# Optimization experiments

Measured on AMD Instinct MI355X. Metric: run time of the kernel, lower is better.

## Reference

```python
import jax, jax.numpy as jnp
import numpy as np

EPS = 0.01    # halting threshold eps
MU = 2.0      # halting probability multiplier
N_MAX = 16    # static upper bound on ACT steps (loop halts in 1-2 steps w/ bias=1, mu=2)

# Binarize: hard threshold at 1-eps forward, straight-through (identity) backward
@jax.custom_vjp
def binarize(x):
    return (x >= 1.0 - EPS).astype(x.dtype)

def _bin_fwd(x):
    return binarize(x), None

def _bin_bwd(_, g):
    return (g,)

binarize.defvjp(_bin_fwd, _bin_bwd)


def setup_inputs() -> dict:
    key = jax.random.key(0)
    ks = jax.random.split(key, 12)
    I, H, O = 4095, 4096, 4096
    sc = 1.0 / np.sqrt(H)
    u = lambda k, s: jax.random.uniform(k, s, jnp.float32, -sc, sc)
    return {
        "x": jax.random.normal(ks[0], (I,), jnp.float32),
        "s0": jax.random.normal(ks[1], (H,), jnp.float32) * 0.1,
        "y0": jax.random.normal(ks[2], (O,), jnp.float32),
        "h0": jnp.zeros((1,), jnp.float32),
        # nn.RNN (tanh) single layer params
        "W_ih": u(ks[3], (H, 1 + I)),
        "b_ih": u(ks[4], (H,)),
        "W_hh": u(ks[5], (H, H)),
        "b_hh": u(ks[6], (H,)),
        # fc_halt (bias hard-set to 1.0 in __init__)
        "W_halt": u(ks[7], (1, H)),
        "b_halt": jnp.ones((1,), jnp.float32),
        # fc_output
        "W_out": u(ks[8], (O, H)),
        "b_out": u(ks[9], (O,)),
    }


def reference(x, s0, y0, h0, W_ih, b_ih, W_hh, b_hh, W_halt, b_halt, W_out, b_out):
    x0 = jnp.concatenate([jnp.zeros((1,), x.dtype), x])  # skip-flag 0 input
    x1 = jnp.concatenate([jnp.ones((1,), x.dtype), x])   # skip-flag 1 input (first step)

    def step(carry, t):
        s, acc = carry
        xin = jnp.where(t == 0, x1, x0)
        valid = acc[0] < 1.0 - EPS  # ACT while-loop condition at step start
        s_new = jnp.tanh(W_ih @ xin + b_ih + W_hh @ s + b_hh)  # tanh RNN cell
        y_new = W_out @ s_new + b_out
        acc_new = acc + MU * jax.nn.sigmoid(W_halt @ s_new + b_halt)
        s_next = jnp.where(valid, s_new, s)
        acc_next = jnp.where(valid, acc_new, acc)
        return (s_next, acc_next), (s_new, y_new, acc_new, valid)

    (_, _), (S, Y, A, V) = jax.lax.scan(step, (s0, h0), jnp.arange(N_MAX))
    # S:[T,H]  Y:[T,O]  A:[T,1]  V:[T] bool
    vmask = V.astype(x.dtype)                 # steps the ACT loop actually executed
    bin_acc = binarize(A[:, 0])               # 0 before halting step, 1 at/after
    halt_bin = bin_acc * vmask                # exactly 1 at the halting step n
    h0_bin = binarize(h0)[0]
    y_sel = jnp.einsum('to,t->o', Y, halt_bin)   # torch.mv(outputs_tensor, bin)
    s_sel = jnp.einsum('th,t->h', S, halt_bin)
    output = h0_bin * y0 + (1.0 - h0_bin) * y_sel
    s = h0_bin * s0 + (1.0 - h0_bin) * s_sel
    ponder = (1.0 - h0_bin) * jnp.sum(vmask * (1.0 - bin_acc))   # = n-1, or 0 if no steps
    last_acc = h0_bin * h0 + (1.0 - h0_bin) * jnp.sum(halt_bin * A[:, 0])[None]
    return (output, s, ponder, last_acc - 1.0)
```

## Files before the change

kernel.cpp:

```cpp
#include <hip/hip_runtime.h>
#include <math.h>


#define H      4096
#define NMAX   16
#define THRESH 0.99f

__device__ __forceinline__ float wave_reduce(float a) {
    #pragma unroll
    for (int off = 32; off > 0; off >>= 1) a += __shfl_down(a, off);
    return a;
}

__global__ __launch_bounds__(256) void k_prep(
    const float* __restrict__ x, float* __restrict__ ws, float* __restrict__ out)
{
    const int i = blockIdx.x * 256 + threadIdx.x;
    if (i < 32) ws[i] = 0.f;
    if (i == 0) out[H] = 0.f;
    if (i < H - 1) out[H + 1 + i] = x[i];
}

__global__ __launch_bounds__(256, 8) void k_step0(
    const float* __restrict__ s0,     const float* __restrict__ h0,
    const float* __restrict__ W_ih,   const float* __restrict__ b_ih,
    const float* __restrict__ W_hh,   const float* __restrict__ b_hh,
    const float* __restrict__ W_halt,
    float* __restrict__ ws, float* __restrict__ out)
{
    if (h0[0] >= THRESH) return;

    const int tid  = threadIdx.x, bid = blockIdx.x;
    const int wave = tid >> 6,   lane = tid & 63;
    const int row  = (bid << 1) + (wave >> 1);
    const int base = ((wave & 1) << 9) + lane;

    const float4* wi4 = (const float4*)(W_ih + (size_t)row * H);
    const float4* wh4 = (const float4*)(W_hh + (size_t)row * H);
    const float4* xv4 = (const float4*)(out + H);
    const float4* sv4 = (const float4*)s0;

    float4 wa[8];
    #pragma unroll
    for (int k = 0; k < 8; ++k) wa[k] = wi4[base + (k << 6)];
    float a0 = 0.f;
    #pragma unroll
    for (int k = 0; k < 8; ++k) {
        float4 xv = xv4[base + (k << 6)];
        a0 += wa[k].x*xv.x + wa[k].y*xv.y + wa[k].z*xv.z + wa[k].w*xv.w;
    }
    float4 wb[8];
    #pragma unroll
    for (int k = 0; k < 8; ++k) wb[k] = wh4[base + (k << 6)];
    float a1 = 0.f;
    #pragma unroll
    for (int k = 0; k < 8; ++k) {
        float4 sv = sv4[base + (k << 6)];
        a1 += wb[k].x*sv.x + wb[k].y*sv.y + wb[k].z*sv.z + wb[k].w*sv.w;
    }

    float a = wave_reduce(a0 + a1);
    __shared__ float part[4];
    if (lane == 0) part[wave] = a;
    __syncthreads();
    if (tid == 0) {
        const int r0 = bid << 1, r1 = r0 + 1;
        float z0 = part[0] + part[1] + b_ih[r0] + b_hh[r0] + W_ih[(size_t)r0 * H];
        float z1 = part[2] + part[3] + b_ih[r1] + b_hh[r1] + W_ih[(size_t)r1 * H];
        float s1a = tanhf(z0), s1b = tanhf(z1);
        ws[32 + r0] = s1a;
        ws[32 + r1] = s1b;
        out[r0] = W_halt[r0] * s1a;
        out[r1] = W_halt[r1] * s1b;
    }
}

#define RG   256
#define RT   256

__device__ __forceinline__ void grid_barrier(int* cnt, int* gen) {
    __syncthreads();
    if (threadIdx.x == 0) {
        __threadfence();
        int g = __hip_atomic_load(gen, __ATOMIC_RELAXED, __HIP_MEMORY_SCOPE_AGENT);
        int prev = __hip_atomic_fetch_add(cnt, 1, __ATOMIC_ACQ_REL, __HIP_MEMORY_SCOPE_AGENT);
        if (prev == RG - 1) {
            __hip_atomic_store(cnt, 0, __ATOMIC_RELAXED, __HIP_MEMORY_SCOPE_AGENT);
            __hip_atomic_fetch_add(gen, 1, __ATOMIC_RELEASE, __HIP_MEMORY_SCOPE_AGENT);
        } else {
            while (__hip_atomic_load(gen, __ATOMIC_ACQUIRE, __HIP_MEMORY_SCOPE_AGENT) == g)
                __builtin_amdgcn_s_sleep(8);
        }
        __threadfence();
    }
    __syncthreads();
}

__global__ __launch_bounds__(RT) void k_rest(
    const float* __restrict__ x,
    const float* __restrict__ h0,
    const float* __restrict__ W_ih,   const float* __restrict__ b_ih,
    const float* __restrict__ W_hh,   const float* __restrict__ b_hh,
    const float* __restrict__ W_halt, const float* __restrict__ b_halt,
    const float* __restrict__ hpart,  float* ws)
{
    int* wsI = (int*)ws;
    if (h0[0] >= THRESH) return;

    const int tid = threadIdx.x, bid = blockIdx.x;
    const int wave = tid >> 6, lane = tid & 63;

    {
        const float4* p4 = (const float4*)hpart;
        float a = 0.f;
        #pragma unroll
        for (int j = 0; j < 4; ++j) {
            float4 v = p4[tid + (j << 8)];
            a += v.x + v.y + v.z + v.w;
        }
        a = wave_reduce(a);
        __shared__ float pr[4];
        if (lane == 0) pr[wave] = a;
        __syncthreads();
        float hd  = pr[0] + pr[1] + pr[2] + pr[3];
        float sg  = 1.f / (1.f + expf(-(hd + b_halt[0])));
        float acc0 = h0[0] + 2.f * sg;
        if (acc0 >= THRESH) {
            if (bid == 0 && tid == 0) {
                wsI[4] = 1; wsI[5] = 0; wsI[6] = 0; ws[8] = acc0;
            }
            return;
        }
        if (bid == 0 && tid == 0) { wsI[4] = 0; }
        __syncthreads();
    }

    float* hdot = ws + 16;
    float* sb0  = ws + 32;
    float* sb1  = ws + 32 + H;

    __shared__ float xl[H];
    __shared__ float sl[H];
    if (tid == 0) xl[0] = 0.f;
    for (int i = tid; i < H - 1; i += RT) xl[i + 1] = x[i];

    float acc;
    {
        const float4* p4 = (const float4*)hpart;
        float a = 0.f;
        #pragma unroll
        for (int j = 0; j < 4; ++j) {
            float4 v = p4[tid + (j << 8)];
            a += v.x + v.y + v.z + v.w;
        }
        a = wave_reduce(a);
        __shared__ float pr2[4];
        if (lane == 0) pr2[wave] = a;
        __syncthreads();
        float hd = pr2[0] + pr2[1] + pr2[2] + pr2[3];
        acc = h0[0] + 2.f / (1.f + expf(-(hd + b_halt[0])));
    }
    int   ponder = 1;
    const float bh = b_halt[0];
    bool  halted = false;
    int   sel = 0;
    float last_acc = 0.f;

    for (int t = 1; t < NMAX; ++t) {
        const float* scur = (t & 1) ? sb0 : sb1;
        float*       snew = (t & 1) ? sb1 : sb0;

        __syncthreads();
        for (int i = tid; i < H / 4; i += RT)
            ((float4*)sl)[i] = ((const float4*)scur)[i];
        __syncthreads();

        for (int r = 0; r < 4; ++r) {
            const int row = bid * 16 + r * 4 + wave;
            const float4* wih = (const float4*)(W_ih + (size_t)row * H);
            const float4* whh = (const float4*)(W_hh + (size_t)row * H);
            float a0 = 0.f, a1 = 0.f;
            #pragma unroll 4
            for (int k = 0; k < 16; ++k) {
                const int idx = lane + (k << 6);
                float4 wa = wih[idx], wb = whh[idx];
                float4 va = ((const float4*)xl)[idx], vb = ((const float4*)sl)[idx];
                a0 += wa.x*va.x + wa.y*va.y + wa.z*va.z + wa.w*va.w;
                a1 += wb.x*vb.x + wb.y*vb.y + wb.z*vb.z + wb.w*vb.w;
            }
            float a = wave_reduce(a0 + a1);
            if (lane == 0) {
                float sv = tanhf(a + b_ih[row] + b_hh[row]);
                snew[row] = sv;
                atomicAdd(&hdot[t], W_halt[row] * sv);
            }
        }

        grid_barrier((int*)ws, (int*)ws + 1);

        float hd = ((volatile float*)hdot)[t];
        float sg = 1.f / (1.f + expf(-(hd + bh)));
        acc += 2.f * sg;
        if (acc >= THRESH) { halted = true; last_acc = acc; sel = (t & 1) ? 1 : 0; break; }
        ponder++;
    }

    if (bid == 0 && tid == 0) {
        wsI[4] = halted ? 1 : 0;
        wsI[5] = sel;
        wsI[6] = ponder;
        ws[8]  = last_acc;
    }
}

__global__ __launch_bounds__(256, 8) void k_out(
    const float* __restrict__ s0,    const float* __restrict__ y0,
    const float* __restrict__ h0,
    const float* __restrict__ W_out, const float* __restrict__ b_out,
    const float* __restrict__ ws, float* __restrict__ out)
{
    const float h0v = h0[0];
    const int tid = threadIdx.x, bid = blockIdx.x;

    if (h0v >= THRESH) {
        const int i = bid * 256 + tid;
        if (i < H) { out[i] = y0[i]; out[H + i] = s0[i]; }
        if (i == 0) { out[2*H] = 0.f; out[2*H + 1] = h0v - 1.f; }
        return;
    }

    const int* wsI = (const int*)ws;
    if (!wsI[4]) {
        const int i = bid * 256 + tid;
        if (i < H) { out[i] = 0.f; out[H + i] = 0.f; }
        if (i == 0) { out[2*H] = (float)wsI[6]; out[2*H + 1] = -1.f; }
        return;
    }

    const float* sfin = ws + 32 + (wsI[5] ? H : 0);
    const int wave = tid >> 6, lane = tid & 63;
    const int row  = (bid << 1) + (wave >> 1);
    const int base = ((wave & 1) << 9) + lane;

    const float4* w4 = (const float4*)(W_out + (size_t)row * H);
    const float4* v4 = (const float4*)sfin;

    float4 wa[8];
    #pragma unroll
    for (int k = 0; k < 8; ++k) wa[k] = w4[base + (k << 6)];
    float a0 = 0.f;
    #pragma unroll
    for (int k = 0; k < 8; ++k) {
        float4 vv = v4[base + (k << 6)];
        a0 += wa[k].x*vv.x + wa[k].y*vv.y + wa[k].z*vv.z + wa[k].w*vv.w;
    }

    float a = wave_reduce(a0);
    __shared__ float part[4];
    if (lane == 0) part[wave] = a;
    __syncthreads();
    if (tid == 0) {
        const int r0 = bid << 1, r1 = r0 + 1;
        out[r0]     = part[0] + part[1] + b_out[r0];
        out[r1]     = part[2] + part[3] + b_out[r1];
        out[H + r0] = sfin[r0];
        out[H + r1] = sfin[r1];
        if (bid == 0) {
            out[2*H]     = (float)wsI[6];
            out[2*H + 1] = ws[8] - 1.f;
        }
    }
}

extern "C" void kernel_launch(void* const* d_in, const int* in_sizes, int n_in,
                              void* d_out, int out_size, void* d_ws, size_t ws_size,
                              hipStream_t stream) {
    const float* x      = (const float*)d_in[0];
    const float* s0     = (const float*)d_in[1];
    const float* y0     = (const float*)d_in[2];
    const float* h0     = (const float*)d_in[3];
    const float* W_ih   = (const float*)d_in[4];
    const float* b_ih   = (const float*)d_in[5];
    const float* W_hh   = (const float*)d_in[6];
    const float* b_hh   = (const float*)d_in[7];
    const float* W_halt = (const float*)d_in[8];
    const float* b_halt = (const float*)d_in[9];
    const float* W_out  = (const float*)d_in[10];
    const float* b_out  = (const float*)d_in[11];
    float* out = (float*)d_out;
    float* ws  = (float*)d_ws;

    k_prep<<<dim3(16),   dim3(256), 0, stream>>>(x, ws, out);
    k_step0<<<dim3(2048), dim3(256), 0, stream>>>(
        s0, h0, W_ih, b_ih, W_hh, b_hh, W_halt, ws, out);
    k_rest<<<dim3(RG),   dim3(RT),  0, stream>>>(
        x, h0, W_ih, b_ih, W_hh, b_hh, W_halt, b_halt, out, ws);
    k_out<<<dim3(2048),  dim3(256), 0, stream>>>(
        s0, y0, h0, W_out, b_out, ws, out);
}
```

Before: 224.6 us.

## Fuse step0, recurrent steps and output projection into one persistent kernel

```diff
diff --git a/kernel.cpp b/kernel.cpp
--- a/kernel.cpp
+++ b/kernel.cpp
@@ -5,78 +5,14 @@
 #define H      4096
 #define NMAX   16
 #define THRESH 0.99f
+#define RG     1024
+#define RT     256
 
 __device__ __forceinline__ float wave_reduce(float a) {
     #pragma unroll
     for (int off = 32; off > 0; off >>= 1) a += __shfl_down(a, off);
     return a;
 }
-
-__global__ __launch_bounds__(256) void k_prep(
-    const float* __restrict__ x, float* __restrict__ ws, float* __restrict__ out)
-{
-    const int i = blockIdx.x * 256 + threadIdx.x;
-    if (i < 32) ws[i] = 0.f;
-    if (i == 0) out[H] = 0.f;
-    if (i < H - 1) out[H + 1 + i] = x[i];
-}
-
-__global__ __launch_bounds__(256, 8) void k_step0(
-    const float* __restrict__ s0,     const float* __restrict__ h0,
-    const float* __restrict__ W_ih,   const float* __restrict__ b_ih,
-    const float* __restrict__ W_hh,   const float* __restrict__ b_hh,
-    const float* __restrict__ W_halt,
-    float* __restrict__ ws, float* __restrict__ out)
-{
-    if (h0[0] >= THRESH) return;
-
-    const int tid  = threadIdx.x, bid = blockIdx.x;
-    const int wave = tid >> 6,   lane = tid & 63;
-    const int row  = (bid << 1) + (wave >> 1);
-    const int base = ((wave & 1) << 9) + lane;
-
-    const float4* wi4 = (const float4*)(W_ih + (size_t)row * H);
-    const float4* wh4 = (const float4*)(W_hh + (size_t)row * H);
-    const float4* xv4 = (const float4*)(out + H);
-    const float4* sv4 = (const float4*)s0;
-
-    float4 wa[8];
-    #pragma unroll
-    for (int k = 0; k < 8; ++k) wa[k] = wi4[base + (k << 6)];
-    float a0 = 0.f;
-    #pragma unroll
-    for (int k = 0; k < 8; ++k) {
-        float4 xv = xv4[base + (k << 6)];
-        a0 += wa[k].x*xv.x + wa[k].y*xv.y + wa[k].z*xv.z + wa[k].w*xv.w;
-    }
-    float4 wb[8];
-    #pragma unroll
-    for (int k = 0; k < 8; ++k) wb[k] = wh4[base + (k << 6)];
-    float a1 = 0.f;
-    #pragma unroll
-    for (int k = 0; k < 8; ++k) {
-        float4 sv = sv4[base + (k << 6)];
-        a1 += wb[k].x*sv.x + wb[k].y*sv.y + wb[k].z*sv.z + wb[k].w*sv.w;
-    }
-
-    float a = wave_reduce(a0 + a1);
-    __shared__ float part[4];
-    if (lane == 0) part[wave] = a;
-    __syncthreads();
-    if (tid == 0) {
-        const int r0 = bid << 1, r1 = r0 + 1;
-        float z0 = part[0] + part[1] + b_ih[r0] + b_hh[r0] + W_ih[(size_t)r0 * H];
-        float z1 = part[2] + part[3] + b_ih[r1] + b_hh[r1] + W_ih[(size_t)r1 * H];
-        float s1a = tanhf(z0), s1b = tanhf(z1);
-        ws[32 + r0] = s1a;
-        ws[32 + r1] = s1b;
-        out[r0] = W_halt[r0] * s1a;
-        out[r1] = W_halt[r1] * s1b;
-    }
-}
-
-#define RG   256
-#define RT   256
 
 __device__ __forceinline__ void grid_barrier(int* cnt, int* gen) {
     __syncthreads();
@@ -96,53 +32,83 @@
     __syncthreads();
 }
 
-__global__ __launch_bounds__(RT) void k_rest(
-    const float* __restrict__ x,
+__global__ __launch_bounds__(256) void k_prep(
+    const float* __restrict__ x, float* __restrict__ ws, float* __restrict__ out)
+{
+    const int i = blockIdx.x * 256 + threadIdx.x;
+    if (i < 32) ws[i] = 0.f;
+    if (i == 0) out[H] = 0.f;
+    if (i < H - 1) out[H + 1 + i] = x[i];
+}
+
+__global__ __launch_bounds__(RT, 4) void k_main(
+    const float* __restrict__ s0,    const float* __restrict__ y0,
     const float* __restrict__ h0,
-    const float* __restrict__ W_ih,   const float* __restrict__ b_ih,
-    const float* __restrict__ W_hh,   const float* __restrict__ b_hh,
-    const float* __restrict__ W_halt, const float* __restrict__ b_halt,
-    const float* __restrict__ hpart,  float* ws)
+    const float* __restrict__ W_ih,  const float* __restrict__ b_ih,
+    const float* __restrict__ W_hh,  const float* __restrict__ b_hh,
+    const float* __restrict__ W_halt,const float* __restrict__ b_halt,
+    const float* __restrict__ W_out, const float* __restrict__ b_out,
+    float* ws, float* __restrict__ out)
 {
-    int* wsI = (int*)ws;
-    if (h0[0] >= THRESH) return;
-
-    const int tid = threadIdx.x, bid = blockIdx.x;
+    const int tid  = threadIdx.x, bid = blockIdx.x;
+    const float h0v = h0[0];
+
+    if (h0v >= THRESH) {
+        const int i = bid * RT + tid;
+        if (i < H) { out[i] = y0[i]; out[H + i] = s0[i]; }
+        if (i == 0) { out[2*H] = 0.f; out[2*H + 1] = h0v - 1.f; }
+        return;
+    }
+
     const int wave = tid >> 6, lane = tid & 63;
+    const int row  = (bid << 2) + wave;
+
+    float* sb0   = ws + 32;
+    float* sb1   = ws + 32 + H;
+    float* hpart = ws + 32 + 2 * H;
+    float* hdot  = ws + 16;
+
+    const float4* wi4 = (const float4*)(W_ih + (size_t)row * H);
+    const float4* wh4 = (const float4*)(W_hh + (size_t)row * H);
+    const float4* xv4 = (const float4*)(out + H);
+    const float4* sv4 = (const float4*)s0;
+
+    const float bi  = b_ih[row];
+    const float bhh = b_hh[row];
+    const float w0c = W_ih[(size_t)row * H];
+    const float whl = W_halt[row];
+    const float bha = b_halt[0];
 
     {
-        const float4* p4 = (const float4*)hpart;
-        float a = 0.f;
+        float a0 = 0.f, a1 = 0.f;
+        float4 wreg[8];
         #pragma unroll
-        for (int j = 0; j < 4; ++j) {
-            float4 v = p4[tid + (j << 8)];
-            a += v.x + v.y + v.z + v.w;
-        }
-        a = wave_reduce(a);
-        __shared__ float pr[4];
-        if (lane == 0) pr[wave] = a;
-        __syncthreads();
-        float hd  = pr[0] + pr[1] + pr[2] + pr[3];
-        float sg  = 1.f / (1.f + expf(-(hd + b_halt[0])));
-        float acc0 = h0[0] + 2.f * sg;
-        if (acc0 >= THRESH) {
-            if (bid == 0 && tid == 0) {
-                wsI[4] = 1; wsI[5] = 0; wsI[6] = 0; ws[8] = acc0;
-            }
-            return;
-        }
-        if (bid == 0 && tid == 0) { wsI[4] = 0; }
-        __syncthreads();
-    }
-
-    float* hdot = ws + 16;
-    float* sb0  = ws + 32;
-    float* sb1  = ws + 32 + H;
-
-    __shared__ float xl[H];
-    __shared__ float sl[H];
-    if (tid == 0) xl[0] = 0.f;
-    for (int i = tid; i < H - 1; i += RT) xl[i + 1] = x[i];
+        for (int hseg = 0; hseg < 2; ++hseg) {
+            const int off = hseg << 9;
+            #pragma unroll
+            for (int k = 0; k < 8; ++k) wreg[k] = wi4[off + lane + (k << 6)];
+            #pragma unroll
+            for (int k = 0; k < 8; ++k) {
+                float4 v = xv4[off + lane + (k << 6)];
+                a0 += wreg[k].x*v.x + wreg[k].y*v.y + wreg[k].z*v.z + wreg[k].w*v.w;
+            }
+            #pragma unroll
+            for (int k = 0; k < 8; ++k) wreg[k] = wh4[off + lane + (k << 6)];
+            #pragma unroll
+            for (int k = 0; k < 8; ++k) {
+                float4 v = sv4[off + lane + (k << 6)];
+                a1 += wreg[k].x*v.x + wreg[k].y*v.y + wreg[k].z*v.z + wreg[k].w*v.w;
+            }
+        }
+        float a = wave_reduce(a0 + a1);
+        if (lane == 0) {
+            float s1 = tanhf(a + bi + bhh + w0c);
+            sb0[row]   = s1;
+            hpart[row] = whl * s1;
+        }
+    }
+
+    grid_barrier((int*)ws, (int*)ws + 1);
 
     float acc;
     {
@@ -154,121 +120,84 @@
             a += v.x + v.y + v.z + v.w;
         }
         a = wave_reduce(a);
-        __shared__ float pr2[4];
-        if (lane == 0) pr2[wave] = a;
+        __shared__ float pr[4];
+        if (lane == 0) pr[wave] = a;
         __syncthreads();
-        float hd = pr2[0] + pr2[1] + pr2[2] + pr2[3];
-        acc = h0[0] + 2.f / (1.f + expf(-(hd + b_halt[0])));
-    }
-    int   ponder = 1;
-    const float bh = b_halt[0];
-    bool  halted = false;
-    int   sel = 0;
-    float last_acc = 0.f;
-
-    for (int t = 1; t < NMAX; ++t) {
-        const float* scur = (t & 1) ? sb0 : sb1;
-        float*       snew = (t & 1) ? sb1 : sb0;
-
-        __syncthreads();
-        for (int i = tid; i < H / 4; i += RT)
-            ((float4*)sl)[i] = ((const float4*)scur)[i];
-        __syncthreads();
-
-        for (int r = 0; r < 4; ++r) {
-            const int row = bid * 16 + r * 4 + wave;
-            const float4* wih = (const float4*)(W_ih + (size_t)row * H);
-            const float4* whh = (const float4*)(W_hh + (size_t)row * H);
+        float hd = pr[0] + pr[1] + pr[2] + pr[3];
+        acc = h0v + 2.f / (1.f + expf(-(hd + bha)));
+    }
+
+    bool  halted;
+    int   sel = 0, ponder = 0;
+    float last_acc;
+
+    if (acc >= THRESH) {
+        halted = true; last_acc = acc;
+    } else {
+        halted = false; last_acc = 0.f; ponder = 1;
+        for (int t = 1; t < NMAX; ++t) {
+            const float* scur = (t & 1) ? sb0 : sb1;
+            float*       snew = (t & 1) ? sb1 : sb0;
+            const float4* sc4 = (const float4*)scur;
+
             float a0 = 0.f, a1 = 0.f;
             #pragma unroll 4
             for (int k = 0; k < 16; ++k) {
                 const int idx = lane + (k << 6);
-                float4 wa = wih[idx], wb = whh[idx];
-                float4 va = ((const float4*)xl)[idx], vb = ((const float4*)sl)[idx];
+                float4 wa = wi4[idx], wb = wh4[idx];
+                float4 va = xv4[idx], vb = sc4[idx];
                 a0 += wa.x*va.x + wa.y*va.y + wa.z*va.z + wa.w*va.w;
                 a1 += wb.x*vb.x + wb.y*vb.y + wb.z*vb.z + wb.w*vb.w;
             }
             float a = wave_reduce(a0 + a1);
             if (lane == 0) {
-                float sv = tanhf(a + b_ih[row] + b_hh[row]);
+                float sv = tanhf(a + bi + bhh);
                 snew[row] = sv;
-                atomicAdd(&hdot[t], W_halt[row] * sv);
-            }
-        }
-
-        grid_barrier((int*)ws, (int*)ws + 1);
-
-        float hd = ((volatile float*)hdot)[t];
-        float sg = 1.f / (1.f + expf(-(hd + bh)));
-        acc += 2.f * sg;
-        if (acc >= THRESH) { halted = true; last_acc = acc; sel = (t & 1) ? 1 : 0; break; }
-        ponder++;
-    }
-
+                atomicAdd(&hdot[t], whl * sv);
+            }
+
+            grid_barrier((int*)ws, (int*)ws + 1);
+
+            float hd = ((volatile float*)hdot)[t];
+            acc += 2.f / (1.f + expf(-(hd + bha)));
+            if (acc >= THRESH) {
+                halted = true; last_acc = acc; sel = (t & 1) ? 1 : 0; break;
+            }
+            ponder++;
+        }
+    }
+
+    if (halted) {
+        const float* sfin = sel ? sb1 : sb0;
+        const float4* wo4 = (const float4*)(W_out + (size_t)row * H);
+        const float4* vf4 = (const float4*)sfin;
+        const float bo = b_out[row];
+
+        float a0 = 0.f, a1 = 0.f;
+        float4 wreg[8];
+        #pragma unroll
+        for (int hseg = 0; hseg < 2; ++hseg) {
+            const int off = hseg << 9;
+            #pragma unroll
+            for (int k = 0; k < 8; ++k) wreg[k] = wo4[off + lane + (k << 6)];
+            #pragma unroll
+            for (int k = 0; k < 8; ++k) {
+                float4 v = vf4[off + lane + (k << 6)];
+                a0 += wreg[k].x*v.x + wreg[k].y*v.y + wreg[k].z*v.z + wreg[k].w*v.w;
+            }
+        }
+        float a = wave_reduce(a0 + a1);
+        if (lane == 0) {
+            out[row]     = a + bo;
+            out[H + row] = sfin[row];
+        }
+    } else {
+        const int i = bid * RT + tid;
+        if (i < H) { out[i] = 0.f; out[H + i] = 0.f; }
+    }
     if (bid == 0 && tid == 0) {
-        wsI[4] = halted ? 1 : 0;
-        wsI[5] = sel;
-        wsI[6] = ponder;
-        ws[8]  = last_acc;
-    }
-}
-
-__global__ __launch_bounds__(256, 8) void k_out(
-    const float* __restrict__ s0,    const float* __restrict__ y0,
-    const float* __restrict__ h0,
-    const float* __restrict__ W_out, const float* __restrict__ b_out,
-    const float* __restrict__ ws, float* __restrict__ out)
-{
-    const float h0v = h0[0];
-    const int tid = threadIdx.x, bid = blockIdx.x;
-
-    if (h0v >= THRESH) {
-        const int i = bid * 256 + tid;
-        if (i < H) { out[i] = y0[i]; out[H + i] = s0[i]; }
-        if (i == 0) { out[2*H] = 0.f; out[2*H + 1] = h0v - 1.f; }
-        return;
-    }
-
-    const int* wsI = (const int*)ws;
-    if (!wsI[4]) {
-        const int i = bid * 256 + tid;
-        if (i < H) { out[i] = 0.f; out[H + i] = 0.f; }
-        if (i == 0) { out[2*H] = (float)wsI[6]; out[2*H + 1] = -1.f; }
-        return;
-    }
-
-    const float* sfin = ws + 32 + (wsI[5] ? H : 0);
-    const int wave = tid >> 6, lane = tid & 63;
-    const int row  = (bid << 1) + (wave >> 1);
-    const int base = ((wave & 1) << 9) + lane;
-
-    const float4* w4 = (const float4*)(W_out + (size_t)row * H);
-    const float4* v4 = (const float4*)sfin;
-
-    float4 wa[8];
-    #pragma unroll
-    for (int k = 0; k < 8; ++k) wa[k] = w4[base + (k << 6)];
-    float a0 = 0.f;
-    #pragma unroll
-    for (int k = 0; k < 8; ++k) {
-        float4 vv = v4[base + (k << 6)];
-        a0 += wa[k].x*vv.x + wa[k].y*vv.y + wa[k].z*vv.z + wa[k].w*vv.w;
-    }
-
-    float a = wave_reduce(a0);
-    __shared__ float part[4];
-    if (lane == 0) part[wave] = a;
-    __syncthreads();
-    if (tid == 0) {
-        const int r0 = bid << 1, r1 = r0 + 1;
-        out[r0]     = part[0] + part[1] + b_out[r0];
-        out[r1]     = part[2] + part[3] + b_out[r1];
-        out[H + r0] = sfin[r0];
-        out[H + r1] = sfin[r1];
-        if (bid == 0) {
-            out[2*H]     = (float)wsI[6];
-            out[2*H + 1] = ws[8] - 1.f;
-        }
+        out[2*H]     = (float)ponder;
+        out[2*H + 1] = halted ? (last_acc - 1.f) : -1.f;
     }
 }
 
@@ -290,11 +219,7 @@
     float* out = (float*)d_out;
     float* ws  = (float*)d_ws;
 
-    k_prep<<<dim3(16),   dim3(256), 0, stream>>>(x, ws, out);
-    k_step0<<<dim3(2048), dim3(256), 0, stream>>>(
-        s0, h0, W_ih, b_ih, W_hh, b_hh, W_halt, ws, out);
-    k_rest<<<dim3(RG),   dim3(RT),  0, stream>>>(
-        x, h0, W_ih, b_ih, W_hh, b_hh, W_halt, b_halt, out, ws);
-    k_out<<<dim3(2048),  dim3(256), 0, stream>>>(
-        s0, y0, h0, W_out, b_out, ws, out);
-}
+    k_prep<<<dim3(16),  dim3(256), 0, stream>>>(x, ws, out);
+    k_main<<<dim3(RG),  dim3(RT),  0, stream>>>(
+        s0, y0, h0, W_ih, b_ih, W_hh, b_hh, W_halt, b_halt, W_out, b_out, ws, out);
+}
```

Result: slower. 453.4 us (+101.9%).
